# Performance work log

Hardware: AMD Instinct MI355X
Metric: run time of the kernel (lower is better)

## Reference

```python
import jax, jax.numpy as jnp
import numpy as np

IN, OUT, B = 8192, 8192, 256

def setup_inputs() -> dict:
    key = jax.random.key(0)
    k1, k2, k3, k4, k5 = jax.random.split(key, 5)
    x = jax.random.normal(k1, (B, IN), dtype=jnp.float32)
    low = jax.random.uniform(k2, (IN,), dtype=jnp.float32, minval=-1.0, maxval=0.0)
    high = low + jax.random.uniform(k3, (IN,), dtype=jnp.float32)  # guarantees low <= high
    W = jax.random.normal(k4, (OUT, IN), dtype=jnp.float32) * 0.02
    b = jax.random.normal(k5, (OUT,), dtype=jnp.float32) * 0.02
    return {"x": x, "low": low, "high": high, "W": W, "b": b}

def reference(x, low, high, W, b):
    # standard linear: x @ W.T + b
    y = jnp.einsum('bi,oi->bo', x, W) + b
    # interval bound propagation: swap bounds where weights are negative.
    # Equivalent to per-row masked matmul loop in the original:
    #   low_out[i]  = (W+[i] @ low) + (W-[i] @ high) + b[i]
    #   high_out[i] = (W+[i] @ high) + (W-[i] @ low) + b[i]
    W_pos = jnp.maximum(W, 0.0)
    W_neg = jnp.minimum(W, 0.0)
    low_out = W_pos @ low + W_neg @ high + b
    high_out = W_pos @ high + W_neg @ low + b
    return (y, low_out, high_out)
```

## Files before the change

### kernel.cpp

```cpp
#include <hip/hip_runtime.h>

#define M_TOTAL 256
#define N_TOTAL 8192
#define K_TOTAL 8192
#define TM 64
#define TN 64
#define BK 64
#define KITERS (K_TOTAL / BK)

typedef __attribute__((ext_vector_type(4))) float f32x4;
typedef __attribute__((ext_vector_type(8))) short s16x8;
typedef __attribute__((ext_vector_type(2))) int i32x2;

__device__ __forceinline__ int pk(float a, float b) {
    return (int)__builtin_amdgcn_perm(__float_as_uint(b), __float_as_uint(a), 0x07060302u);
}

__device__ __forceinline__ void barrier_lds() {
    asm volatile("s_waitcnt lgkmcnt(0)\n\ts_barrier" ::: "memory");
}

__global__ __launch_bounds__(256, 2)
void abstract_linear_kernel(const float* __restrict__ x,
                            const float* __restrict__ low,
                            const float* __restrict__ high,
                            const float* __restrict__ W,
                            const float* __restrict__ bias,
                            float* __restrict__ out) {
    __shared__ __align__(16) unsigned short As[2][TM * BK];
    __shared__ __align__(16) unsigned short Bs[2][TN * BK];

    const int t  = threadIdx.x;
    const int bx = blockIdx.x;
    const int n0 = (bx & 127) * TN;
    const int m_tile = bx >> 7;
    const int m0 = m_tile * TM;
    const bool do_bounds = (m_tile == 0);

    const int g  = t >> 4;
    const int sg = t & 15;

    const float* xg = x + (size_t)(m0 + g) * K_TOTAL + sg * 4;
    const float* wg = W + (size_t)(n0 + g) * K_TOTAL + sg * 4;
    const float* lg = low  + sg * 4;
    const float* hg = high + sg * 4;

    const int wave = t >> 6;
    const int lane = t & 63;
    const int wm  = wave >> 1;
    const int wn  = wave & 1;
    const int l15 = lane & 15;
    const int lq  = lane >> 4;

    f32x4 acc[2][2];
#pragma unroll
    for (int i = 0; i < 2; ++i)
#pragma unroll
        for (int j = 0; j < 2; ++j)
            acc[i][j] = (f32x4){0.f, 0.f, 0.f, 0.f};

    float P[4] = {0.f, 0.f, 0.f, 0.f};
    float R[4] = {0.f, 0.f, 0.f, 0.f};

    f32x4 a_reg[2][4], w_reg[2][4], lo_reg[2], hi_reg[2];

    auto issue = [&](int sl, int it) {
        const int kb = it * BK;
#pragma unroll
        for (int j = 0; j < 4; ++j)
            a_reg[sl][j] = *(const f32x4*)(xg + (size_t)j * 16 * K_TOTAL + kb);
#pragma unroll
        for (int j = 0; j < 4; ++j)
            w_reg[sl][j] = *(const f32x4*)(wg + (size_t)j * 16 * K_TOTAL + kb);
        if (do_bounds) {
            lo_reg[sl] = *(const f32x4*)(lg + kb);
            hi_reg[sl] = *(const f32x4*)(hg + kb);
        }
    };

    const int a_chunk = sg >> 1;
    const int a_half  = sg & 1;

    auto convert_write = [&](int sl, int buf) {
#pragma unroll
        for (int j = 0; j < 4; ++j) {
            f32x4 u = a_reg[sl][j];
            i32x2 d;
            d[0] = pk(u[0], u[1]);
            d[1] = pk(u[2], u[3]);
            int row = j * 16 + g;
            int pos = a_chunk ^ (row & 7);
            *(i32x2*)&As[buf][row * BK + pos * 8 + a_half * 4] = d;
        }
#pragma unroll
        for (int j = 0; j < 4; ++j) {
            f32x4 u = w_reg[sl][j];
            i32x2 d;
            d[0] = pk(u[0], u[1]);
            d[1] = pk(u[2], u[3]);
            int row = j * 16 + g;
            int pos = a_chunk ^ (row & 7);
            *(i32x2*)&Bs[buf][row * BK + pos * 8 + a_half * 4] = d;
        }
        if (do_bounds) {
            f32x4 l = lo_reg[sl], h = hi_reg[sl];
#pragma unroll
            for (int j = 0; j < 4; ++j) {
                f32x4 w = w_reg[sl][j];
#pragma unroll
                for (int e = 0; e < 4; ++e) {
                    float wv = w[e];
                    P[j] = fmaf(wv,        l[e] + h[e], P[j]);
                    R[j] = fmaf(fabsf(wv), h[e] - l[e], R[j]);
                }
            }
        }
    };

    auto mfma_tile = [&](int buf) {
#pragma unroll
        for (int s = 0; s < 2; ++s) {
            s16x8 af[2], bf[2];
#pragma unroll
            for (int mi = 0; mi < 2; ++mi) {
                int row = wm * 32 + mi * 16 + l15;
                int pos = (s * 4 + lq) ^ (row & 7);
                af[mi] = *(const s16x8*)&As[buf][row * BK + pos * 8];
            }
#pragma unroll
            for (int ni = 0; ni < 2; ++ni) {
                int row = wn * 32 + ni * 16 + l15;
                int pos = (s * 4 + lq) ^ (row & 7);
                bf[ni] = *(const s16x8*)&Bs[buf][row * BK + pos * 8];
            }
#pragma unroll
            for (int mi = 0; mi < 2; ++mi)
#pragma unroll
                for (int ni = 0; ni < 2; ++ni)
                    acc[mi][ni] = __builtin_amdgcn_mfma_f32_16x16x32_bf16(
                        af[mi], bf[ni], acc[mi][ni], 0, 0, 0);
        }
    };

    issue(0, 0);
    issue(1, 1);
    convert_write(0, 0);
    barrier_lds();

    for (int it = 0; it < KITERS - 2; it += 2) {
        issue(0, it + 2);
        mfma_tile(0);
        convert_write(1, 1);
        barrier_lds();

        issue(1, it + 3);
        mfma_tile(1);
        convert_write(0, 0);
        barrier_lds();
    }
    mfma_tile(0);
    convert_write(1, 1);
    barrier_lds();
    mfma_tile(1);

#pragma unroll
    for (int ni = 0; ni < 2; ++ni) {
        int go = n0 + wn * 32 + ni * 16 + l15;
        float bv = bias[go];
#pragma unroll
        for (int mi = 0; mi < 2; ++mi) {
            int gr = m0 + wm * 32 + mi * 16 + lq * 4;
#pragma unroll
            for (int r = 0; r < 4; ++r)
                out[(size_t)(gr + r) * N_TOTAL + go] = acc[mi][ni][r] + bv;
        }
    }

    if (do_bounds) {
#pragma unroll
        for (int j = 0; j < 4; ++j) {
            float p = P[j], r = R[j];
            p += __shfl_xor(p, 1);
            p += __shfl_xor(p, 2);
            p += __shfl_xor(p, 4);
            p += __shfl_xor(p, 8);
            r += __shfl_xor(r, 1);
            r += __shfl_xor(r, 2);
            r += __shfl_xor(r, 4);
            r += __shfl_xor(r, 8);
            if (sg == 0) {
                int o = n0 + j * 16 + g;
                float bv = bias[o];
                out[(size_t)M_TOTAL * N_TOTAL + o]           = 0.5f * (p - r) + bv;
                out[(size_t)M_TOTAL * N_TOTAL + N_TOTAL + o] = 0.5f * (p + r) + bv;
            }
        }
    }
}

extern "C" void kernel_launch(void* const* d_in, const int* in_sizes, int n_in,
                              void* d_out, int out_size, void* d_ws, size_t ws_size,
                              hipStream_t stream) {
    const float* x    = (const float*)d_in[0];
    const float* low  = (const float*)d_in[1];
    const float* high = (const float*)d_in[2];
    const float* W    = (const float*)d_in[3];
    const float* b    = (const float*)d_in[4];
    float* out = (float*)d_out;

    dim3 grid(4 * (N_TOTAL / TN));
    dim3 block(256);
    hipLaunchKernelGGL(abstract_linear_kernel, grid, block, 0, stream,
                       x, low, high, W, b, out);
}
```

Baseline: 440.8 us.

## Pre-convert x to swizzled bf16, use 128-row tiles with split-K waves

Adds a prep kernel that converts x to bf16 in a pre-swizzled LDS-ready layout and precomputes low+high and high-low vectors. The main kernel uses 128x64 tiles split across two K-halves per block (waves handle separate K ranges), reducing the number of W re-reads from four M-tiles to two, and distributes bound-propagation work across all blocks instead of only m_tile 0. Partial sums are combined through shared memory at the end. This trades an extra launch, workspace traffic and lower occupancy (256 blocks, 1 per CU) for less redundant W loading and conversion.

```diff
diff --git a/kernel.cpp b/kernel.cpp
--- a/kernel.cpp
+++ b/kernel.cpp
@@ -3,14 +3,15 @@
 #define M_TOTAL 256
 #define N_TOTAL 8192
 #define K_TOTAL 8192
-#define TM 64
+#define TM 128
 #define TN 64
 #define BK 64
-#define KITERS (K_TOTAL / BK)
+#define PH 64
 
 typedef __attribute__((ext_vector_type(4))) float f32x4;
 typedef __attribute__((ext_vector_type(8))) short s16x8;
-typedef __attribute__((ext_vector_type(2))) int i32x2;
+typedef __attribute__((ext_vector_type(4))) int   i32x4;
+typedef unsigned short ushort_t;
 
 __device__ __forceinline__ int pk(float a, float b) {
     return (int)__builtin_amdgcn_perm(__float_as_uint(b), __float_as_uint(a), 0x07060302u);
@@ -20,140 +21,167 @@
     asm volatile("s_waitcnt lgkmcnt(0)\n\ts_barrier" ::: "memory");
 }
 
-__global__ __launch_bounds__(256, 2)
-void abstract_linear_kernel(const float* __restrict__ x,
-                            const float* __restrict__ low,
-                            const float* __restrict__ high,
+__global__ __launch_bounds__(256)
+void prep_kernel(const float* __restrict__ x,
+                 const float* __restrict__ low,
+                 const float* __restrict__ high,
+                 ushort_t* __restrict__ xpre,
+                 float* __restrict__ lhv,
+                 float* __restrict__ hlv) {
+    const int bx = blockIdx.x, t = threadIdx.x;
+    if (bx < 1024) {
+        const int gid = bx * 256 + t;
+        const int ci  = gid & 1023;
+        const int p   = (gid >> 10) & 63;
+        const int khh = (gid >> 16) & 1;
+        const int mtt = gid >> 17;
+        const int row = ci >> 3;
+        const int kc  = (ci & 7) ^ (row & 7);
+        const float* src = x + (size_t)(mtt * 128 + row) * K_TOTAL
+                             + khh * 4096 + p * 64 + kc * 8;
+        f32x4 s0 = *(const f32x4*)(src);
+        f32x4 s1 = *(const f32x4*)(src + 4);
+        i32x4 bi;
+        bi[0] = pk(s0[0], s0[1]); bi[1] = pk(s0[2], s0[3]);
+        bi[2] = pk(s1[0], s1[1]); bi[3] = pk(s1[2], s1[3]);
+        *(i32x4*)(xpre + (size_t)gid * 8) = bi;
+    } else {
+        const int i = (bx - 1024) * 256 + t;
+        float lo = low[i], hi = high[i];
+        lhv[i] = lo + hi;
+        hlv[i] = hi - lo;
+    }
+}
+
+__global__ __launch_bounds__(256, 1)
+void abstract_linear_kernel(const ushort_t* __restrict__ xpre,
                             const float* __restrict__ W,
+                            const float* __restrict__ lh,
+                            const float* __restrict__ hl,
                             const float* __restrict__ bias,
                             float* __restrict__ out) {
-    __shared__ __align__(16) unsigned short As[2][TM * BK];
-    __shared__ __align__(16) unsigned short Bs[2][TN * BK];
-
-    const int t  = threadIdx.x;
-    const int bx = blockIdx.x;
-    const int n0 = (bx & 127) * TN;
-    const int m_tile = bx >> 7;
-    const int m0 = m_tile * TM;
-    const bool do_bounds = (m_tile == 0);
-
-    const int g  = t >> 4;
-    const int sg = t & 15;
-
-    const float* xg = x + (size_t)(m0 + g) * K_TOTAL + sg * 4;
-    const float* wg = W + (size_t)(n0 + g) * K_TOTAL + sg * 4;
-    const float* lg = low  + sg * 4;
-    const float* hg = high + sg * 4;
-
+    __shared__ __align__(16) ushort_t As[2][2][TM * BK];
+    __shared__ __align__(16) ushort_t Bs[2][2][TN * BK];
+    __shared__ float ybuf[TM * TN];
+    __shared__ float pbuf[2][TN];
+    __shared__ float rbuf[2][TN];
+
+    const int t    = threadIdx.x;
+    const int bx   = blockIdx.x;
+    const int nt   = bx & 127;
+    const int mt   = bx >> 7;
+    const int n0   = nt * TN;
     const int wave = t >> 6;
+    const int m    = wave & 1;
+    const int kh   = wave >> 1;
     const int lane = t & 63;
-    const int wm  = wave >> 1;
-    const int wn  = wave & 1;
-    const int l15 = lane & 15;
-    const int lq  = lane >> 4;
-
-    f32x4 acc[2][2];
-#pragma unroll
-    for (int i = 0; i < 2; ++i)
-#pragma unroll
-        for (int j = 0; j < 2; ++j)
+    const int l15  = lane & 15;
+    const int lq   = lane >> 4;
+    const int tt   = t & 127;
+    const int trow = tt >> 3;
+    const int tk   = tt & 7;
+
+    f32x4 acc[4][4];
+#pragma unroll
+    for (int i = 0; i < 4; ++i)
+#pragma unroll
+        for (int j = 0; j < 4; ++j)
             acc[i][j] = (f32x4){0.f, 0.f, 0.f, 0.f};
 
-    float P[4] = {0.f, 0.f, 0.f, 0.f};
-    float R[4] = {0.f, 0.f, 0.f, 0.f};
-
-    f32x4 a_reg[2][4], w_reg[2][4], lo_reg[2], hi_reg[2];
-
-    auto issue = [&](int sl, int it) {
-        const int kb = it * BK;
-#pragma unroll
-        for (int j = 0; j < 4; ++j)
-            a_reg[sl][j] = *(const f32x4*)(xg + (size_t)j * 16 * K_TOTAL + kb);
-#pragma unroll
-        for (int j = 0; j < 4; ++j)
-            w_reg[sl][j] = *(const f32x4*)(wg + (size_t)j * 16 * K_TOTAL + kb);
-        if (do_bounds) {
-            lo_reg[sl] = *(const f32x4*)(lg + kb);
-            hi_reg[sl] = *(const f32x4*)(hg + kb);
-        }
-    };
-
-    const int a_chunk = sg >> 1;
-    const int a_half  = sg & 1;
+    const int jb = mt * 2;
+    float P[2] = {0.f, 0.f};
+    float R[2] = {0.f, 0.f};
+
+    const float*    wgp = W + (size_t)(n0 + trow) * K_TOTAL + kh * 4096 + tk * 8;
+    const float*    lhp = lh + kh * 4096 + tk * 8;
+    const float*    hlp = hl + kh * 4096 + tk * 8;
+    const ushort_t* ap  = xpre + (size_t)(mt * 2 + kh) * PH * (TM * BK) + tt * 8;
+
+    i32x4 areg[2][8];
+    f32x4 wreg[2][8];
+    f32x4 lhreg[2][2], hlreg[2][2];
+
+    auto issueA = [&](int sl, int p) {
+        const ushort_t* a_p = ap + (size_t)p * (TM * BK);
+#pragma unroll
+        for (int jj = 0; jj < 8; ++jj)
+            areg[sl][jj] = *(const i32x4*)(a_p + jj * 1024);
+    };
+    auto issueW = [&](int sl, int p) {
+        const float* w_p = wgp + p * BK;
+#pragma unroll
+        for (int j = 0; j < 4; ++j) {
+            wreg[sl][j * 2]     = *(const f32x4*)(w_p + (size_t)j * 16 * K_TOTAL);
+            wreg[sl][j * 2 + 1] = *(const f32x4*)(w_p + (size_t)j * 16 * K_TOTAL + 4);
+        }
+        lhreg[sl][0] = *(const f32x4*)(lhp + p * BK);
+        lhreg[sl][1] = *(const f32x4*)(lhp + p * BK + 4);
+        hlreg[sl][0] = *(const f32x4*)(hlp + p * BK);
+        hlreg[sl][1] = *(const f32x4*)(hlp + p * BK + 4);
+    };
+
+    const int cwc = (tk ^ (trow & 7)) * 8;
 
     auto convert_write = [&](int sl, int buf) {
 #pragma unroll
+        for (int jj = 0; jj < 8; ++jj)
+            *(i32x4*)&As[kh][buf][jj * 1024 + tt * 8] = areg[sl][jj];
+#pragma unroll
         for (int j = 0; j < 4; ++j) {
-            f32x4 u = a_reg[sl][j];
-            i32x2 d;
-            d[0] = pk(u[0], u[1]);
-            d[1] = pk(u[2], u[3]);
-            int row = j * 16 + g;
-            int pos = a_chunk ^ (row & 7);
-            *(i32x2*)&As[buf][row * BK + pos * 8 + a_half * 4] = d;
-        }
-#pragma unroll
-        for (int j = 0; j < 4; ++j) {
-            f32x4 u = w_reg[sl][j];
-            i32x2 d;
-            d[0] = pk(u[0], u[1]);
-            d[1] = pk(u[2], u[3]);
-            int row = j * 16 + g;
-            int pos = a_chunk ^ (row & 7);
-            *(i32x2*)&Bs[buf][row * BK + pos * 8 + a_half * 4] = d;
-        }
-        if (do_bounds) {
-            f32x4 l = lo_reg[sl], h = hi_reg[sl];
-#pragma unroll
-            for (int j = 0; j < 4; ++j) {
-                f32x4 w = w_reg[sl][j];
-#pragma unroll
-                for (int e = 0; e < 4; ++e) {
-                    float wv = w[e];
-                    P[j] = fmaf(wv,        l[e] + h[e], P[j]);
-                    R[j] = fmaf(fabsf(wv), h[e] - l[e], R[j]);
-                }
+            f32x4 u0 = wreg[sl][j * 2], u1 = wreg[sl][j * 2 + 1];
+            i32x4 d;
+            d[0] = pk(u0[0], u0[1]); d[1] = pk(u0[2], u0[3]);
+            d[2] = pk(u1[0], u1[1]); d[3] = pk(u1[2], u1[3]);
+            *(i32x4*)&Bs[kh][buf][(j * 16 + trow) * BK + cwc] = d;
+        }
+#pragma unroll
+        for (int jj = 0; jj < 2; ++jj) {
+            f32x4 w0 = wreg[sl][(jb + jj) * 2], w1 = wreg[sl][(jb + jj) * 2 + 1];
+            f32x4 lA = lhreg[sl][0], lB = lhreg[sl][1];
+            f32x4 hA = hlreg[sl][0], hB = hlreg[sl][1];
+#pragma unroll
+            for (int e = 0; e < 4; ++e) {
+                P[jj] = fmaf(w0[e], lA[e], P[jj]);
+                P[jj] = fmaf(w1[e], lB[e], P[jj]);
+                R[jj] = fmaf(fabsf(w0[e]), hA[e], R[jj]);
+                R[jj] = fmaf(fabsf(w1[e]), hB[e], R[jj]);
             }
         }
     };
 
+    const int sw = l15 & 7;
     auto mfma_tile = [&](int buf) {
 #pragma unroll
         for (int s = 0; s < 2; ++s) {
-            s16x8 af[2], bf[2];
-#pragma unroll
-            for (int mi = 0; mi < 2; ++mi) {
-                int row = wm * 32 + mi * 16 + l15;
-                int pos = (s * 4 + lq) ^ (row & 7);
-                af[mi] = *(const s16x8*)&As[buf][row * BK + pos * 8];
-            }
-#pragma unroll
-            for (int ni = 0; ni < 2; ++ni) {
-                int row = wn * 32 + ni * 16 + l15;
-                int pos = (s * 4 + lq) ^ (row & 7);
-                bf[ni] = *(const s16x8*)&Bs[buf][row * BK + pos * 8];
-            }
-#pragma unroll
-            for (int mi = 0; mi < 2; ++mi)
-#pragma unroll
-                for (int ni = 0; ni < 2; ++ni)
+            const int pos = ((s * 4 + lq) ^ sw) * 8;
+            s16x8 af[4], bf[4];
+#pragma unroll
+            for (int mi = 0; mi < 4; ++mi)
+                af[mi] = *(const s16x8*)&As[kh][buf][(m * 64 + mi * 16 + l15) * BK + pos];
+#pragma unroll
+            for (int ni = 0; ni < 4; ++ni)
+                bf[ni] = *(const s16x8*)&Bs[kh][buf][(ni * 16 + l15) * BK + pos];
+#pragma unroll
+            for (int mi = 0; mi < 4; ++mi)
+#pragma unroll
+                for (int ni = 0; ni < 4; ++ni)
                     acc[mi][ni] = __builtin_amdgcn_mfma_f32_16x16x32_bf16(
                         af[mi], bf[ni], acc[mi][ni], 0, 0, 0);
         }
     };
 
-    issue(0, 0);
-    issue(1, 1);
+    issueA(0, 0); issueW(0, 0);
+    issueA(1, 1); issueW(1, 1);
     convert_write(0, 0);
     barrier_lds();
 
-    for (int it = 0; it < KITERS - 2; it += 2) {
-        issue(0, it + 2);
+    for (int p = 0; p < PH - 2; p += 2) {
+        issueA(0, p + 2); issueW(0, p + 2);
         mfma_tile(0);
         convert_write(1, 1);
         barrier_lds();
 
-        issue(1, it + 3);
+        issueA(1, p + 3); issueW(1, p + 3);
         mfma_tile(1);
         convert_write(0, 0);
         barrier_lds();
@@ -164,37 +192,52 @@
     mfma_tile(1);
 
 #pragma unroll
-    for (int ni = 0; ni < 2; ++ni) {
-        int go = n0 + wn * 32 + ni * 16 + l15;
-        float bv = bias[go];
-#pragma unroll
-        for (int mi = 0; mi < 2; ++mi) {
-            int gr = m0 + wm * 32 + mi * 16 + lq * 4;
-#pragma unroll
-            for (int r = 0; r < 4; ++r)
-                out[(size_t)(gr + r) * N_TOTAL + go] = acc[mi][ni][r] + bv;
-        }
-    }
-
-    if (do_bounds) {
-#pragma unroll
-        for (int j = 0; j < 4; ++j) {
-            float p = P[j], r = R[j];
-            p += __shfl_xor(p, 1);
-            p += __shfl_xor(p, 2);
-            p += __shfl_xor(p, 4);
-            p += __shfl_xor(p, 8);
-            r += __shfl_xor(r, 1);
-            r += __shfl_xor(r, 2);
-            r += __shfl_xor(r, 4);
-            r += __shfl_xor(r, 8);
-            if (sg == 0) {
-                int o = n0 + j * 16 + g;
-                float bv = bias[o];
-                out[(size_t)M_TOTAL * N_TOTAL + o]           = 0.5f * (p - r) + bv;
-                out[(size_t)M_TOTAL * N_TOTAL + N_TOTAL + o] = 0.5f * (p + r) + bv;
-            }
-        }
+    for (int jj = 0; jj < 2; ++jj) {
+        float p2 = P[jj], r2 = R[jj];
+        p2 += __shfl_xor(p2, 1); p2 += __shfl_xor(p2, 2); p2 += __shfl_xor(p2, 4);
+        r2 += __shfl_xor(r2, 1); r2 += __shfl_xor(r2, 2); r2 += __shfl_xor(r2, 4);
+        if ((lane & 7) == 0) {
+            pbuf[kh][(jb + jj) * 16 + trow] = p2;
+            rbuf[kh][(jb + jj) * 16 + trow] = r2;
+        }
+    }
+
+    if (kh == 0) {
+#pragma unroll
+        for (int mi = 0; mi < 4; ++mi)
+#pragma unroll
+            for (int ni = 0; ni < 4; ++ni)
+#pragma unroll
+                for (int r = 0; r < 4; ++r)
+                    ybuf[(m * 64 + mi * 16 + lq * 4 + r) * TN + ni * 16 + l15] =
+                        acc[mi][ni][r];
+    }
+    __syncthreads();
+
+    if (kh == 1) {
+        float bv[4];
+#pragma unroll
+        for (int ni = 0; ni < 4; ++ni) bv[ni] = bias[n0 + ni * 16 + l15];
+#pragma unroll
+        for (int mi = 0; mi < 4; ++mi)
+#pragma unroll
+            for (int ni = 0; ni < 4; ++ni)
+#pragma unroll
+                for (int r = 0; r < 4; ++r) {
+                    int lrow = m * 64 + mi * 16 + lq * 4 + r;
+                    float v = acc[mi][ni][r] + ybuf[lrow * TN + ni * 16 + l15];
+                    out[(size_t)(mt * TM + lrow) * N_TOTAL + n0 + ni * 16 + l15] =
+                        v + bv[ni];
+                }
+    }
+
+    if (t < 32) {
+        int row = mt * 32 + t;
+        float Ps = pbuf[0][row] + pbuf[1][row];
+        float Rs = rbuf[0][row] + rbuf[1][row];
+        float bb = bias[n0 + row];
+        out[(size_t)M_TOTAL * N_TOTAL + n0 + row]           = 0.5f * (Ps - Rs) + bb;
+        out[(size_t)M_TOTAL * N_TOTAL + N_TOTAL + n0 + row] = 0.5f * (Ps + Rs) + bb;
     }
 }
 
@@ -208,8 +251,12 @@
     const float* b    = (const float*)d_in[4];
     float* out = (float*)d_out;
 
-    dim3 grid(4 * (N_TOTAL / TN));
-    dim3 block(256);
-    hipLaunchKernelGGL(abstract_linear_kernel, grid, block, 0, stream,
-                       x, low, high, W, b, out);
-}
+    ushort_t* xpre = (ushort_t*)d_ws;
+    float* lhv = (float*)((char*)d_ws + (size_t)M_TOTAL * K_TOTAL * 2);
+    float* hlv = lhv + K_TOTAL;
+
+    hipLaunchKernelGGL(prep_kernel, dim3(1056), dim3(256), 0, stream,
+                       x, low, high, xpre, lhv, hlv);
+    hipLaunchKernelGGL(abstract_linear_kernel, dim3(256), dim3(256), 0, stream,
+                       xpre, W, lhv, hlv, b, out);
+}
```

Result: slower. 646.5 us (+46.7%).
